# Performance work log

Hardware: AMD Instinct MI355X
Metric: run time of the kernel (lower is better)

Reference implementation:

```python
import jax, jax.numpy as jnp
import numpy as np

DIM = 1024
HEADS = 16
HEAD_DIM = DIM // HEADS

def setup_inputs() -> dict:
    key = jax.random.key(0)
    ks = jax.random.split(key, 5)
    x = jax.random.normal(ks[0], (4, 2048, DIM), dtype=jnp.float32)
    s = DIM ** -0.5
    W_qkv = jax.random.normal(ks[1], (DIM, 3 * DIM), dtype=jnp.float32) * s
    b_qkv = jnp.zeros((3 * DIM,), dtype=jnp.float32)
    W_proj = jax.random.normal(ks[2], (DIM, DIM), dtype=jnp.float32) * s
    b_proj = jnp.zeros((DIM,), dtype=jnp.float32)
    return {"x": x, "W_qkv": W_qkv, "b_qkv": b_qkv, "W_proj": W_proj, "b_proj": b_proj}

def reference(x, W_qkv, b_qkv, W_proj, b_proj):
    B, S, D = x.shape
    scale = HEAD_DIM ** -0.5
    qkv = x @ W_qkv + b_qkv                      # [B,S,3D]
    q, k, v = jnp.split(qkv, 3, axis=-1)         # each [B,S,D]
    def heads(t):
        return t.reshape(B, S, HEADS, HEAD_DIM).transpose(0, 2, 1, 3)  # [B,H,S,d]
    q, k, v = heads(q), heads(k), heads(v)
    attn = jnp.einsum('bhqd,bhkd->bhqk', q, k) * scale
    attn = jax.nn.softmax(attn, axis=-1)
    out = jnp.einsum('bhqk,bhkd->bhqd', attn, v)  # [B,H,S,d]
    out = out.transpose(0, 2, 1, 3).reshape(B, S, D)
    return out @ W_proj + b_proj
```

## Files before the change

### kernel.cpp

```cpp
#include <hip/hip_runtime.h>
#include <hip/hip_bf16.h>
#include <cstdint>


#define SEQ   2048
#define NDIM  1024
#define HEADS 16
#define HD    64

typedef __attribute__((ext_vector_type(8))) short bf16x8;
typedef __attribute__((ext_vector_type(4))) float f32x4;

typedef __attribute__((address_space(1))) void glob_void;
typedef __attribute__((address_space(3))) void lds_void;

__device__ __forceinline__ short f2b(float f) {
    uint32_t u = __float_as_uint(f);
    u += 0x7FFF + ((u >> 16) & 1);
    return (short)(u >> 16);
}
__device__ __forceinline__ uint32_t cvtpk(float lo, float hi) {
    uint32_t d;
    asm("v_cvt_pk_bf16_f32 %0, %1, %2" : "=v"(d) : "v"(lo), "v"(hi));
    return d;
}

__global__ __launch_bounds__(256) void sentinel_k(float* __restrict__ out, float v, int n) {
    const int i = blockIdx.x * 256 + threadIdx.x;
    if (i < n) out[i] = v;
}

__global__ __launch_bounds__(256) void convert_k(const float* __restrict__ in,
                                                 short* __restrict__ out, int n8) {
    const int i = blockIdx.x * 256 + threadIdx.x;
    if (i >= n8) return;
    const float4 f0 = *(const float4*)(in + (size_t)i * 8);
    const float4 f1 = *(const float4*)(in + (size_t)i * 8 + 4);
    union { bf16x8 v; short s[8]; } u;
    u.s[0] = f2b(f0.x); u.s[1] = f2b(f0.y); u.s[2] = f2b(f0.z); u.s[3] = f2b(f0.w);
    u.s[4] = f2b(f1.x); u.s[5] = f2b(f1.y); u.s[6] = f2b(f1.z); u.s[7] = f2b(f1.w);
    *(bf16x8*)(out + (size_t)i * 8) = u.v;
}

__global__ __launch_bounds__(256) void transpose_k(const float* __restrict__ W,
                                                   short* __restrict__ WT,
                                                   int R, int C) {
    __shared__ short t[32][33];
    const int bx = blockIdx.x * 32;
    const int by = blockIdx.y * 32;
    const int tx = threadIdx.x, ty = threadIdx.y;
#pragma unroll
    for (int i = 0; i < 32; i += 8)
        t[ty + i][tx] = f2b(W[(size_t)(by + ty + i) * C + bx + tx]);
    __syncthreads();
#pragma unroll
    for (int i = 0; i < 32; i += 8)
        WT[(size_t)(bx + ty + i) * R + by + tx] = t[tx][ty + i];
}

__global__ __launch_bounds__(256) void gemm_bt(const void* __restrict__ A,
                                               const short* __restrict__ BT,
                                               const float* __restrict__ bias,
                                               void* __restrict__ Cout,
                                               int N, int K, int lda,
                                               int amode, int cmode) {
    __shared__ short As[128 * 64];
    __shared__ short Bs[128 * 64];

    const short* Ab = (const short*)A;
    const float* Af = (const float*)A;

    const int tid  = threadIdx.x;
    const int lane = tid & 63;
    const int wid  = tid >> 6;
    const int ln16 = lane & 15;
    const int quad = lane >> 4;
    const int wm = (wid & 1) * 64;
    const int wn = (wid >> 1) * 64;

    const int nbx = gridDim.x;
    const int nby = gridDim.y;
    const int nwg = nbx * nby;
    const int lin = blockIdx.y * nbx + blockIdx.x;
    int bm, bn;
    if ((nwg & 7) == 0 && (nbx & 3) == 0 && (nby & 3) == 0) {
        const int cpx = nwg >> 3;
        const int g   = (lin & 7) * cpx + (lin >> 3);
        const int s   = g >> 4;
        const int t   = g & 15;
        const int nsx = nbx >> 2;
        const int sx  = s % nsx;
        const int sy  = s / nsx;
        bn = ((sx << 2) + (t & 3)) * 128;
        bm = ((sy << 2) + (t >> 2)) * 128;
    } else {
        bm = blockIdx.y * 128;
        bn = blockIdx.x * 128;
    }

    f32x4 acc[4][4];
#pragma unroll
    for (int i = 0; i < 4; ++i)
#pragma unroll
        for (int j = 0; j < 4; ++j) {
            acc[i][j][0] = 0.f; acc[i][j][1] = 0.f; acc[i][j][2] = 0.f; acc[i][j][3] = 0.f;
        }

    const int rbase = tid >> 3;
    const int k8    = (tid & 7) * 8;

    for (int ks = 0; ks < K; ks += 64) {
        __syncthreads();
#pragma unroll
        for (int i = 0; i < 4; ++i) {
            const int row = i * 32 + rbase;
            const int c   = i * 256 + tid;
            const short* gb = BT + (size_t)(bn + row) * K + ks + k8;
            __builtin_amdgcn_global_load_lds((glob_void*)gb, (lds_void*)(Bs + c * 8), 16, 0, 0);
        }
        if (amode) {
#pragma unroll
            for (int i = 0; i < 4; ++i) {
                const int row = i * 32 + rbase;
                const int c   = i * 256 + tid;
                const short* ga = Ab + (size_t)(bm + row) * lda + ks + k8;
                __builtin_amdgcn_global_load_lds((glob_void*)ga, (lds_void*)(As + c * 8), 16, 0, 0);
            }
        } else {
#pragma unroll
            for (int i = 0; i < 4; ++i) {
                const int row = i * 32 + rbase;
                const int c   = i * 256 + tid;
                const float* ga = Af + (size_t)(bm + row) * lda + ks + k8;
                const float4 f0 = *(const float4*)ga;
                const float4 f1 = *(const float4*)(ga + 4);
                union { bf16x8 v; short s[8]; } u;
                u.s[0] = f2b(f0.x); u.s[1] = f2b(f0.y); u.s[2] = f2b(f0.z); u.s[3] = f2b(f0.w);
                u.s[4] = f2b(f1.x); u.s[5] = f2b(f1.y); u.s[6] = f2b(f1.z); u.s[7] = f2b(f1.w);
                *(bf16x8*)(As + c * 8) = u.v;
            }
        }
        __syncthreads();

#pragma unroll
        for (int kk = 0; kk < 2; ++kk) {
            bf16x8 a[4], b[4];
#pragma unroll
            for (int t = 0; t < 4; ++t) {
                a[t] = *(const bf16x8*)(As + (wm + t * 16 + ln16) * 64 + kk * 32 + quad * 8);
                b[t] = *(const bf16x8*)(Bs + (wn + t * 16 + ln16) * 64 + kk * 32 + quad * 8);
            }
#pragma unroll
            for (int tm = 0; tm < 4; ++tm)
#pragma unroll
                for (int tn = 0; tn < 4; ++tn)
                    acc[tm][tn] = __builtin_amdgcn_mfma_f32_16x16x32_bf16(a[tm], b[tn], acc[tm][tn], 0, 0, 0);
        }
    }

#pragma unroll
    for (int tm = 0; tm < 4; ++tm) {
        const int row = bm + wm + tm * 16 + quad * 4;
#pragma unroll
        for (int tn = 0; tn < 4; ++tn) {
            const int col = bn + wn + tn * 16 + ln16;
            const float bv = bias[col];
#pragma unroll
            for (int r = 0; r < 4; ++r) {
                const float cv = acc[tm][tn][r] + bv;
                const size_t idx = (size_t)(row + r) * N + col;
                if (cmode) ((float*)Cout)[idx] = cv;
                else       ((short*)Cout)[idx] = f2b(cv);
            }
        }
    }
}

__global__ __launch_bounds__(256, 3) void attn_k(short* qkv) {
    __shared__ __attribute__((aligned(16))) char smem[49152];
    short*    Ks   = (short*)smem;
    uint32_t* VTw  = (uint32_t*)(smem + 16384);
    uint32_t* Psw  = (uint32_t*)(smem + 32768);
    short*    Ps   = (short*)(smem + 32768);
    float*    Obuf = (float*)smem;
    float*    lred = (float*)(smem + 32768);

    const int tid  = threadIdx.x;
    const int lane = tid & 63;
    const int wid  = tid >> 6;
    const int ln16 = lane & 15;
    const int quad = lane >> 4;
    const int sw   = ln16 & 7;

    const int i0  = blockIdx.x;
    const int xcd = i0 & 7;
    const int qt  = (i0 >> 3) & 31;
    const int bh  = (i0 >> 8) * 8 + xcd;
    const int b   = bh >> 4;
    const int h   = bh & 15;
    const int q0  = qt * 64;

    const size_t row0 = ((size_t)b * SEQ) * 3072 + h * HD;

#pragma unroll
    for (int i = 0; i < 2; ++i) {
        const int c   = i * 256 + tid;
        const int r   = c >> 3;
        const int col = (c ^ r) & 7;
        __builtin_amdgcn_global_load_lds(
            (glob_void*)(qkv + row0 + (size_t)(q0 + r) * 3072 + col * 8),
            (lds_void*)(Ps + c * 8), 16, 0, 0);
    }
    __syncthreads();
    bf16x8 qf[4][2];
#pragma unroll
    for (int qg = 0; qg < 4; ++qg) {
        const short* qb = Ps + (qg * 16 + ln16) * 64;
        qf[qg][0] = *(const bf16x8*)(qb + ((quad ^ sw) << 3));
        qf[qg][1] = *(const bf16x8*)(qb + (((4 + quad) ^ sw) << 3));
    }
    __syncthreads();

    float l[4] = {0.f, 0.f, 0.f, 0.f};
    f32x4 o[4][4];
#pragma unroll
    for (int t = 0; t < 4; ++t)
#pragma unroll
        for (int qg = 0; qg < 4; ++qg) {
            o[t][qg][0] = 0.f; o[t][qg][1] = 0.f; o[t][qg][2] = 0.f; o[t][qg][3] = 0.f;
        }

    const int vp   = tid & 63;
    const int vd16 = (tid >> 6) * 16;
    const int slab = wid * 32;

    const float C1 = 0.18033688f;
    const float C0 = -17.3123405f;

    for (int kb = 0; kb < SEQ; kb += 128) {
        __syncthreads();
#pragma unroll
        for (int i = 0; i < 4; ++i) {
            const int c   = i * 256 + tid;
            const int r   = c >> 3;
            const int col = (c ^ r) & 7;
            __builtin_amdgcn_global_load_lds(
                (glob_void*)(qkv + row0 + (size_t)(kb + r) * 3072 + 1024 + col * 8),
                (lds_void*)(Ks + c * 8), 16, 0, 0);
        }
        {
            const short* gv = qkv + row0 + (size_t)(kb + 2 * vp) * 3072 + 2048 + vd16;
            union { uint4 u; uint32_t w[4]; } a0, a1, b0, b1;
            a0.u = *(const uint4*)gv;
            a1.u = *(const uint4*)(gv + 8);
            b0.u = *(const uint4*)(gv + 3072);
            b1.u = *(const uint4*)(gv + 3072 + 8);
#pragma unroll
            for (int j = 0; j < 8; ++j) {
                const uint32_t sel = (j & 1) ? 0x07060302u : 0x05040100u;
                const int wsw = vp ^ (j << 2);
                VTw[(vd16 + j) * 64 + wsw]     = __builtin_amdgcn_perm(b0.w[j >> 1], a0.w[j >> 1], sel);
                VTw[(vd16 + 8 + j) * 64 + wsw] = __builtin_amdgcn_perm(b1.w[j >> 1], a1.w[j >> 1], sel);
            }
        }
        __syncthreads();

#pragma unroll
        for (int kg = 0; kg < 2; ++kg) {
            const short* kb_ = Ks + (slab + kg * 16 + ln16) * 64;
            const bf16x8 a0 = *(const bf16x8*)(kb_ + ((quad ^ sw) << 3));
            const bf16x8 a1 = *(const bf16x8*)(kb_ + (((4 + quad) ^ sw) << 3));
#pragma unroll
            for (int qg = 0; qg < 4; ++qg) {
                f32x4 z; z[0] = 0.f; z[1] = 0.f; z[2] = 0.f; z[3] = 0.f;
                z = __builtin_amdgcn_mfma_f32_16x16x32_bf16(a0, qf[qg][0], z, 0, 0, 0);
                z = __builtin_amdgcn_mfma_f32_16x16x32_bf16(a1, qf[qg][1], z, 0, 0, 0);
                const float p0 = __builtin_amdgcn_exp2f(fmaf(z[0], C1, C0));
                const float p1 = __builtin_amdgcn_exp2f(fmaf(z[1], C1, C0));
                const float p2 = __builtin_amdgcn_exp2f(fmaf(z[2], C1, C0));
                const float p3 = __builtin_amdgcn_exp2f(fmaf(z[3], C1, C0));
                l[qg] += (p0 + p1) + (p2 + p3);
                const int prow = qg * 16 + ln16;
                const int wb   = wid * 16 + kg * 8 + quad * 2;
                uint2 pv;
                pv.x = cvtpk(p0, p1);
                pv.y = cvtpk(p2, p3);
                *(uint2*)(Psw + prow * 64 + (wb ^ (sw << 2))) = pv;
            }
        }

        bf16x8 bp[4];
#pragma unroll
        for (int qg = 0; qg < 4; ++qg) {
            const int prow = qg * 16 + ln16;
            bp[qg] = *(const bf16x8*)(Psw + prow * 64 + ((wid * 16 + quad * 4) ^ (sw << 2)));
        }
#pragma unroll
        for (int t = 0; t < 4; ++t) {
            const bf16x8 av = *(const bf16x8*)(VTw + (t * 16 + ln16) * 64
                                               + ((wid * 16 + quad * 4) ^ (sw << 2)));
#pragma unroll
            for (int qg = 0; qg < 4; ++qg)
                o[t][qg] = __builtin_amdgcn_mfma_f32_16x16x32_bf16(av, bp[qg], o[t][qg], 0, 0, 0);
        }
    }

    __syncthreads();
#pragma unroll
    for (int qg = 0; qg < 4; ++qg) {
        l[qg] += __shfl_xor(l[qg], 16, 64);
        l[qg] += __shfl_xor(l[qg], 32, 64);
    }
    if (quad == 0) {
#pragma unroll
        for (int qg = 0; qg < 4; ++qg)
            lred[wid * 64 + qg * 16 + ln16] = l[qg];
    }
    for (int w = 0; w < 4; ++w) {
        if (wid == w) {
#pragma unroll
            for (int t = 0; t < 4; ++t)
#pragma unroll
                for (int qg = 0; qg < 4; ++qg) {
                    float* dst = &Obuf[(qg * 16 + ln16) * 68 + t * 16 + quad * 4];
                    if (w == 0) {
                        *(f32x4*)dst = o[t][qg];
                    } else {
                        f32x4 prev = *(const f32x4*)dst;
                        prev[0] += o[t][qg][0]; prev[1] += o[t][qg][1];
                        prev[2] += o[t][qg][2]; prev[3] += o[t][qg][3];
                        *(f32x4*)dst = prev;
                    }
                }
        }
        __syncthreads();
    }

    const int q  = tid & 63;
    const int dc = (tid >> 6) * 16;
    const float linv = 1.0f / (lred[q] + lred[64 + q] + lred[128 + q] + lred[192 + q]);
    const float* ob = Obuf + q * 68 + dc;
    const f32x4 o0 = *(const f32x4*)ob;
    const f32x4 o1 = *(const f32x4*)(ob + 4);
    const f32x4 o2 = *(const f32x4*)(ob + 8);
    const f32x4 o3 = *(const f32x4*)(ob + 12);
    union { uint4 u[2]; uint32_t w[8]; } outp;
    outp.w[0] = cvtpk(o0[0] * linv, o0[1] * linv);
    outp.w[1] = cvtpk(o0[2] * linv, o0[3] * linv);
    outp.w[2] = cvtpk(o1[0] * linv, o1[1] * linv);
    outp.w[3] = cvtpk(o1[2] * linv, o1[3] * linv);
    outp.w[4] = cvtpk(o2[0] * linv, o2[1] * linv);
    outp.w[5] = cvtpk(o2[2] * linv, o2[3] * linv);
    outp.w[6] = cvtpk(o3[0] * linv, o3[1] * linv);
    outp.w[7] = cvtpk(o3[2] * linv, o3[3] * linv);
    uint4* dst = (uint4*)(qkv + row0 + (size_t)(q0 + q) * 3072 + dc);
    dst[0] = outp.u[0];
    dst[1] = outp.u[1];
}

extern "C" void kernel_launch(void* const* d_in, const int* in_sizes, int n_in,
                              void* d_out, int out_size, void* d_ws, size_t ws_size,
                              hipStream_t stream) {
    const float* x     = (const float*)d_in[0];
    const float* Wqkv  = (const float*)d_in[1];
    const float* bqkv  = (const float*)d_in[2];
    const float* Wproj = (const float*)d_in[3];
    const float* bproj = (const float*)d_in[4];
    float* out = (float*)d_out;

    int bad = -1;
    if (n_in != 5) bad = 9;
    else {
        const int want[5] = {8388608, 3145728, 3072, 1048576, 1024};
        for (int i = 0; i < 5; ++i) if (in_sizes[i] != want[i]) { bad = i; break; }
        if (bad < 0 && out_size != 8388608) bad = 8;
    }
    if (bad >= 0) {
        sentinel_k<<<(out_size + 255) / 256, 256, 0, stream>>>(out, 1000.0f + 100.0f * bad, out_size);
        return;
    }

    char* ws = (char*)d_ws;
    short* wqkvT  = (short*)(ws);
    short* wprojT = (short*)(ws + 6291456);
    short* qkv    = (short*)(ws + 8388608);
    short* xb     = (short*)(ws + 58720256);
    const bool have_xb = (ws_size >= 58720256ull + 16777216ull);

    transpose_k<<<dim3(96, 32), dim3(32, 8), 0, stream>>>(Wqkv, wqkvT, 1024, 3072);
    transpose_k<<<dim3(32, 32), dim3(32, 8), 0, stream>>>(Wproj, wprojT, 1024, 1024);

    if (have_xb) {
        convert_k<<<4096, 256, 0, stream>>>(x, xb, 1048576);
        gemm_bt<<<dim3(3072 / 128, 8192 / 128), 256, 0, stream>>>(
            xb, wqkvT, bqkv, qkv, 3072, 1024, 1024, 1, 0);
    } else {
        gemm_bt<<<dim3(3072 / 128, 8192 / 128), 256, 0, stream>>>(
            x, wqkvT, bqkv, qkv, 3072, 1024, 1024, 0, 0);
    }

    attn_k<<<dim3(4 * HEADS * (SEQ / 64)), 256, 0, stream>>>(qkv);

    gemm_bt<<<dim3(1024 / 128, 8192 / 128), 256, 0, stream>>>(
        qkv, wprojT, bproj, out, 1024, 1024, 3072, 1, 1);
}
```

Measured before the change: 316.1 us.

## Add 256x256-tile double-buffered bf16 GEMM for QKV projection

Adds a new GEMM kernel with 256x256 output tiles, 512 threads and double-buffered LDS loads via global_load_lds, used for the QKV projection when the bf16 copy of x is available. Larger tiles raise arithmetic intensity and cut global traffic per FLOP, and the double buffering overlaps the next K-slice load with MFMA work. It also remaps workgroup IDs in groups of 8 for cache locality. In exchange it uses 128KB of LDS and a large accumulator set, limiting occupancy to one block per CU, and the grid has only 384 blocks.

```diff
diff --git a/kernel.cpp b/kernel.cpp
--- a/kernel.cpp
+++ b/kernel.cpp
@@ -172,6 +172,110 @@
                 if (cmode) ((float*)Cout)[idx] = cv;
                 else       ((short*)Cout)[idx] = f2b(cv);
             }
+        }
+    }
+}
+
+__global__ __launch_bounds__(512, 1) void gemm256_bt(const short* __restrict__ A,
+                                                     const short* __restrict__ BT,
+                                                     const float* __restrict__ bias,
+                                                     short* __restrict__ Cout,
+                                                     int N, int K, int lda) {
+    __shared__ short As2[2][256 * 64];
+    __shared__ short Bs2[2][256 * 64];
+
+    const int tid  = threadIdx.x;
+    const int lane = tid & 63;
+    const int wid  = tid >> 6;
+    const int ln16 = lane & 15;
+    const int quad = lane >> 4;
+    const int wmh  = wid >> 2;
+    const int wnq  = wid & 3;
+
+    const int nbx = gridDim.x;
+    const int nwg = gridDim.x * gridDim.y;
+    int lin = blockIdx.y * nbx + blockIdx.x;
+    if ((nwg & 7) == 0)
+        lin = (lin & 7) * (nwg >> 3) + (lin >> 3);
+    const int bm = (lin / nbx) * 256;
+    const int bn = (lin % nbx) * 256;
+
+    f32x4 acc[8][4];
+#pragma unroll
+    for (int m = 0; m < 8; ++m)
+#pragma unroll
+        for (int n = 0; n < 4; ++n) {
+            acc[m][n][0] = 0.f; acc[m][n][1] = 0.f; acc[m][n][2] = 0.f; acc[m][n][3] = 0.f;
+        }
+
+#pragma unroll
+    for (int i = 0; i < 4; ++i) {
+        const int c  = i * 512 + tid;
+        const int r  = c >> 3;
+        const int k8 = (c & 7) * 8;
+        __builtin_amdgcn_global_load_lds(
+            (glob_void*)(A + (size_t)(bm + r) * lda + k8),
+            (lds_void*)(&As2[0][c * 8]), 16, 0, 0);
+        __builtin_amdgcn_global_load_lds(
+            (glob_void*)(BT + (size_t)(bn + r) * K + k8),
+            (lds_void*)(&Bs2[0][c * 8]), 16, 0, 0);
+    }
+    __syncthreads();
+
+    const int nsteps = K >> 6;
+    for (int t = 0; t < nsteps; ++t) {
+        const int cur = t & 1;
+        const short* Ac = As2[cur];
+        const short* Bc = Bs2[cur];
+
+        if (t + 1 < nsteps) {
+            short* An = As2[cur ^ 1];
+            short* Bn = Bs2[cur ^ 1];
+            const int ko = (t + 1) * 64;
+#pragma unroll
+            for (int i = 0; i < 4; ++i) {
+                const int c  = i * 512 + tid;
+                const int r  = c >> 3;
+                const int k8 = (c & 7) * 8;
+                __builtin_amdgcn_global_load_lds(
+                    (glob_void*)(A + (size_t)(bm + r) * lda + ko + k8),
+                    (lds_void*)(An + c * 8), 16, 0, 0);
+                __builtin_amdgcn_global_load_lds(
+                    (glob_void*)(BT + (size_t)(bn + r) * K + ko + k8),
+                    (lds_void*)(Bn + c * 8), 16, 0, 0);
+            }
+        }
+
+#pragma unroll
+        for (int kk = 0; kk < 2; ++kk) {
+            bf16x8 bf[4];
+#pragma unroll
+            for (int n = 0; n < 4; ++n)
+                bf[n] = *(const bf16x8*)(Bc + (wnq * 64 + n * 16 + ln16) * 64 + kk * 32 + quad * 8);
+            bf16x8 af[8];
+#pragma unroll
+            for (int m = 0; m < 8; ++m)
+                af[m] = *(const bf16x8*)(Ac + (wmh * 128 + m * 16 + ln16) * 64 + kk * 32 + quad * 8);
+#pragma unroll
+            for (int m = 0; m < 8; ++m)
+#pragma unroll
+                for (int n = 0; n < 4; ++n)
+                    acc[m][n] = __builtin_amdgcn_mfma_f32_16x16x32_bf16(af[m], bf[n], acc[m][n], 0, 0, 0);
+        }
+
+        __syncthreads();
+    }
+
+#pragma unroll
+    for (int m = 0; m < 8; ++m) {
+        const int row = bm + wmh * 128 + m * 16 + quad * 4;
+#pragma unroll
+        for (int n = 0; n < 4; ++n) {
+            const int col = bn + wnq * 64 + n * 16 + ln16;
+            const float bv = bias[col];
+#pragma unroll
+            for (int r = 0; r < 4; ++r)
+                Cout[(size_t)(row + r) * N + col] = f2b(acc[m][n][r] + bv);
         }
     }
 }
@@ -392,8 +496,8 @@
 
     if (have_xb) {
         convert_k<<<4096, 256, 0, stream>>>(x, xb, 1048576);
-        gemm_bt<<<dim3(3072 / 128, 8192 / 128), 256, 0, stream>>>(
-            xb, wqkvT, bqkv, qkv, 3072, 1024, 1024, 1, 0);
+        gemm256_bt<<<dim3(3072 / 256, 8192 / 256), 512, 0, stream>>>(
+            xb, wqkvT, bqkv, qkv, 3072, 1024, 1024);
     } else {
         gemm_bt<<<dim3(3072 / 128, 8192 / 128), 256, 0, stream>>>(
             x, wqkvT, bqkv, qkv, 3072, 1024, 1024, 0, 0);
```

Result: slower. 333.1 us (+5.4%).
